# Performance work log

Measured on AMD Instinct MI355X. Metric: run time of the kernel, lower is better.

## Reference

```python
import jax, jax.numpy as jnp
import numpy as np

N, C, CI, H, W = 4, 512, 256, 64, 64  # batch, in_channels, inter_channels, spatial
EPS = 1e-5


def conv1x1(x, w, b):
    # x: (N,C,H,W), w: (O,C), b: (O,)
    return jnp.einsum('nchw,oc->nohw', x, w) + b[None, :, None, None]


def setup_inputs() -> dict:
    key = jax.random.key(0)
    ks = jax.random.split(key, 11)
    s = 0.02
    return {
        'x': jax.random.normal(ks[0], (N, C, H, W), dtype=jnp.float32),
        'g_w': jax.random.normal(ks[1], (CI, C), dtype=jnp.float32) * s,
        'g_b': jax.random.normal(ks[2], (CI,), dtype=jnp.float32) * s,
        'theta_w': jax.random.normal(ks[3], (CI, C), dtype=jnp.float32) * s,
        'theta_b': jax.random.normal(ks[4], (CI,), dtype=jnp.float32) * s,
        'phi_w': jax.random.normal(ks[5], (CI, C), dtype=jnp.float32) * s,
        'phi_b': jax.random.normal(ks[6], (CI,), dtype=jnp.float32) * s,
        'wz_w': jax.random.normal(ks[7], (C, CI), dtype=jnp.float32) * s,
        'wz_b': jax.random.normal(ks[8], (C,), dtype=jnp.float32) * s,
        'bn_gamma': jax.random.normal(ks[9], (C,), dtype=jnp.float32) * 0.1 + 1.0,
        'bn_beta': jax.random.normal(ks[10], (C,), dtype=jnp.float32) * 0.1,
    }


def reference(x, g_w, g_b, theta_w, theta_b, phi_w, phi_b, wz_w, wz_b, bn_gamma, bn_beta):
    # NLBlockND.forward_self, mode='embedded', dimension=2, bn_layer=True
    n = x.shape[0]
    L = x.shape[2] * x.shape[3]  # H*W tokens
    g_x = conv1x1(x, g_w, g_b).reshape(n, CI, L)          # (N,Ci,L)
    theta_x = conv1x1(x, theta_w, theta_b).reshape(n, CI, L)
    phi_x = conv1x1(x, phi_w, phi_b).reshape(n, CI, L)
    f = jnp.einsum('ncl,ncm->nlm', theta_x, phi_x)        # (N,L,L) = theta^T @ phi
    f_div_C = jax.nn.softmax(f, axis=-1)
    y = jnp.einsum('nlm,ncm->ncl', f_div_C, g_x)          # (N,Ci,L) = (attn @ g)^T
    y = y.reshape(n, CI, x.shape[2], x.shape[3])
    w_y = conv1x1(y, wz_w, wz_b)                          # (N,C,H,W)
    # BatchNorm2d, training-mode batch statistics (biased variance)
    mean = jnp.mean(w_y, axis=(0, 2, 3), keepdims=True)
    var = jnp.var(w_y, axis=(0, 2, 3), keepdims=True)
    w_y = (w_y - mean) * jax.lax.rsqrt(var + EPS)
    w_y = w_y * bn_gamma[None, :, None, None] + bn_beta[None, :, None, None]
    return w_y + x
```

## Files before the change

kernel.cpp:

```cpp
#include <hip/hip_runtime.h>
#include <hip/hip_bf16.h>
#include <hip/hip_fp16.h>


#define NB    4
#define CDIM  512
#define CIDIM 256
#define LDIM  4096
#define BN_EPS 1e-5f

typedef unsigned short u16;
typedef __attribute__((ext_vector_type(8))) short short8;
typedef __attribute__((ext_vector_type(4))) float f32x4;
typedef __attribute__((ext_vector_type(16))) float f32x16;

#define WY_OFF    0
#define THPH_OFF  8388608
#define G_OFF     12582912
#define Y_OFF     14680064
#define WTS_OFF   16777216
#define BIAS2_OFF 17039360
#define ML_OFF    17039872
#define ST_OFF    17105408

__device__ __forceinline__ u16 f2b(float f) {
    union { float f; unsigned u; } v; v.f = f;
    return (u16)((v.u + 0x7FFFu + ((v.u >> 16) & 1u)) >> 16);
}

__device__ __forceinline__ float b2f(u16 x) {
    return __uint_as_float((unsigned)x << 16);
}

__device__ __forceinline__ unsigned pack2(float a, float b) {
    return (unsigned)f2b(a) | ((unsigned)f2b(b) << 16);
}

__device__ __forceinline__ void gl_lds16(const u16* g, u16* l) {
    __builtin_amdgcn_global_load_lds(
        (const __attribute__((address_space(1))) void*)g,
        (__attribute__((address_space(3))) void*)l, 16, 0, 0);
}

__global__ void transpose_x(const float* __restrict__ x, u16* __restrict__ xt) {
    __shared__ float tile[32][33];
    int n = blockIdx.z;
    int l0 = blockIdx.x * 32, c0 = blockIdx.y * 32;
    const float* xn = x + (size_t)n * CDIM * LDIM;
    u16* xtn = xt + (size_t)n * LDIM * CDIM;
    int tx = threadIdx.x, ty = threadIdx.y;
#pragma unroll
    for (int k = 0; k < 4; k++)
        tile[ty + 8 * k][tx] = xn[(size_t)(c0 + ty + 8 * k) * LDIM + l0 + tx];
    __syncthreads();
#pragma unroll
    for (int k = 0; k < 4; k++)
        xtn[(size_t)(l0 + ty + 8 * k) * CDIM + c0 + tx] = f2b(tile[tx][ty + 8 * k]);
}

__global__ void cast_w(const float* __restrict__ gw, const float* __restrict__ tw,
                       const float* __restrict__ pw, const float* __restrict__ zw,
                       u16* __restrict__ out) {
    int idx = blockIdx.x * 256 + threadIdx.x;
    if (idx >= 4 * 131072) return;
    int seg = idx >> 17, off = idx & 131071;
    const float* s = (seg == 0) ? gw : (seg == 1) ? tw : (seg == 2) ? pw : zw;
    out[idx] = f2b(s[off]);
}

__global__ void concat_bias(const float* __restrict__ tb, const float* __restrict__ pb,
                            float* __restrict__ out) {
    int i = blockIdx.x * 256 + threadIdx.x;
    if (i < 256) out[i] = tb[i];
    else if (i < 512) out[i] = pb[i - 256];
}

template <int BIAS_MODE, bool OUT_BF16>
__global__ __launch_bounds__(256)
void gemm_nt(const u16* __restrict__ A, const u16* __restrict__ B,
             void* __restrict__ Dv, const float* __restrict__ bias,
             int K, int lda, int ldb, int ldd,
             long batchA, long batchB, long batchD) {
    __shared__ __align__(16) u16 As[128 * 32];
    __shared__ __align__(16) u16 Bs[128 * 32];
    int z = blockIdx.z;
    A += (size_t)z * batchA;
    B += (size_t)z * batchB;

    int tid = threadIdx.x, lane = tid & 63, wave = tid >> 6;
    int n0 = blockIdx.x * 128, m0 = blockIdx.y * 128;
    int wr = wave >> 1, wc = wave & 1;

    f32x4 acc[4][4];
#pragma unroll
    for (int i = 0; i < 4; i++)
#pragma unroll
        for (int j = 0; j < 4; j++) acc[i][j] = (f32x4){0.f, 0.f, 0.f, 0.f};

    int sr = wave * 16 + (lane >> 2);
    int ss = ((lane & 3) ^ ((lane >> 2) & 3)) * 8;
    const u16* Ag0 = A + (size_t)(m0 + sr) * lda + ss;
    const u16* Ag1 = A + (size_t)(m0 + 64 + sr) * lda + ss;
    const u16* Bg0 = B + (size_t)(n0 + sr) * ldb + ss;
    const u16* Bg1 = B + (size_t)(n0 + 64 + sr) * ldb + ss;
    u16* Al0 = &As[(wave * 16) * 32];
    u16* Al1 = &As[(64 + wave * 16) * 32];
    u16* Bl0 = &Bs[(wave * 16) * 32];
    u16* Bl1 = &Bs[(64 + wave * 16) * 32];

    int koff = ((lane >> 4) ^ (lane & 3)) * 8;
    int ra = (wr * 64 + (lane & 15)) * 32 + koff;
    int rb = (wc * 64 + (lane & 15)) * 32 + koff;

    for (int k0 = 0; k0 < K; k0 += 32) {
        __syncthreads();
        gl_lds16(Ag0 + k0, Al0);
        gl_lds16(Ag1 + k0, Al1);
        gl_lds16(Bg0 + k0, Bl0);
        gl_lds16(Bg1 + k0, Bl1);
        __syncthreads();

        short8 af[4], bf[4];
#pragma unroll
        for (int mt = 0; mt < 4; mt++) af[mt] = *(const short8*)&As[ra + mt * 16 * 32];
#pragma unroll
        for (int nt = 0; nt < 4; nt++) bf[nt] = *(const short8*)&Bs[rb + nt * 16 * 32];
#pragma unroll
        for (int mt = 0; mt < 4; mt++)
#pragma unroll
            for (int nt = 0; nt < 4; nt++)
                acc[mt][nt] = __builtin_amdgcn_mfma_f32_16x16x32_bf16(
                    af[mt], bf[nt], acc[mt][nt], 0, 0, 0);
    }

#pragma unroll
    for (int mt = 0; mt < 4; mt++) {
        int mg = m0 + wr * 64 + mt * 16 + (lane >> 4) * 4;
#pragma unroll
        for (int nt = 0; nt < 4; nt++) {
            int ng = n0 + wc * 64 + nt * 16 + (lane & 15);
#pragma unroll
            for (int r = 0; r < 4; r++) {
                float v = acc[mt][nt][r];
                if (BIAS_MODE == 1) v += bias[mg + r];
                if (BIAS_MODE == 2) v += bias[ng];
                if (OUT_BF16) {
                    u16* D = (u16*)Dv + (size_t)z * batchD;
                    D[(size_t)(mg + r) * ldd + ng] = f2b(v);
                } else {
                    float* D = (float*)Dv + (size_t)z * batchD;
                    D[(size_t)(mg + r) * ldd + ng] = v;
                }
            }
        }
    }
}

__global__ __launch_bounds__(256, 2)
void flash_attn(const u16* __restrict__ THPH, const u16* __restrict__ G,
                u16* __restrict__ OPB, unsigned* __restrict__ ML4) {
    __shared__ __align__(16) u16 Ks[2][32 * 256];
    __shared__ __align__(16) u16 Vs[2][256 * 32];

    int b = blockIdx.x;
    int n = b & 3;
    int jh = (b >> 2) & 3;
    int qt = b >> 4;
    int q0 = qt * 128;

    const u16* TH = THPH + (size_t)n * LDIM * 512;
    const u16* PH = TH + 256;
    const u16* Gn = G + (size_t)n * LDIM * CIDIM;
    u16* OPh = OPB + ((size_t)jh * NB + n) * CIDIM * LDIM;
    unsigned* MLh = ML4 + ((size_t)jh * NB + n) * LDIM;

    int tid = threadIdx.x, lane = tid & 63, w = tid >> 6;
    int h = lane >> 5, lq = lane & 31, l7 = lane & 7;

    short8 qf[16];
    {
        const u16* qb = TH + (size_t)(q0 + w * 32 + lq) * 512 + h * 8;
#pragma unroll
        for (int c = 0; c < 16; c++) qf[c] = *(const short8*)(qb + c * 16);
    }

    f32x16 o[8];
#pragma unroll
    for (int i = 0; i < 8; i++)
#pragma unroll
        for (int e = 0; e < 16; e++) o[i][e] = 0.f;
    float m = -3e38f, lsum = 0.f;

    int krh = lane >> 5;
    int ksl = lane & 31;
    int vr = lane >> 2;
    int vsl = (lane & 3) ^ ((lane >> 3) & 3);

#define STAGE(bufi, jt_) do {                                                  \
    int j0_ = jh * 1024 + (jt_) * 32;                                          \
    _Pragma("unroll")                                                          \
    for (int i = 0; i < 4; i++) {                                              \
        int r = w * 8 + 2 * i + krh;                                           \
        int s = ksl ^ (r & 7);                                                 \
        gl_lds16(PH + (size_t)(j0_ + r) * 512 + s * 8,                         \
                 &Ks[bufi][(w * 8 + 2 * i) * 256]);                            \
    }                                                                          \
    _Pragma("unroll")                                                          \
    for (int i = 0; i < 4; i++) {                                              \
        int r = w * 64 + 16 * i + vr;                                          \
        gl_lds16(Gn + (size_t)r * LDIM + j0_ + vsl * 8,                        \
                 &Vs[bufi][(w * 64 + 16 * i) * 32]);                           \
    }                                                                          \
} while (0)

    STAGE(0, 0);
    int cur = 0;

#pragma unroll 1
    for (int jt = 0; jt < 32; jt++) {
        __syncthreads();
        if (jt + 1 < 32) STAGE(cur ^ 1, jt + 1);

        const u16* kb = Ks[cur];
        const u16* vb = Vs[cur];

        f32x16 sv;
#pragma unroll
        for (int e = 0; e < 16; e++) sv[e] = 0.f;
#pragma unroll
        for (int c = 0; c < 16; c++) {
            int slot = (c * 2 + h) ^ l7;
            short8 ka = *(const short8*)&kb[lq * 256 + slot * 8];
            sv = __builtin_amdgcn_mfma_f32_32x32x16_bf16(ka, qf[c], sv, 0, 0, 0);
        }

        float tm = sv[0];
#pragma unroll
        for (int r = 1; r < 16; r++) tm = fmaxf(tm, sv[r]);
        tm = fmaxf(tm, __shfl_xor(tm, 32, 64));

        if (!__all(tm <= m + 8.0f)) {
            float mnew = fmaxf(m, tm);
            float al = __expf(m - mnew);
            m = mnew;
            lsum *= al;
#pragma unroll
            for (int i = 0; i < 8; i++)
#pragma unroll
                for (int e = 0; e < 16; e++) o[i][e] *= al;
        }

        float rs = 0.f;
#pragma unroll
        for (int r = 0; r < 16; r++) {
            float p = __expf(sv[r] - m);
            sv[r] = p;
            rs += p;
        }
        lsum += rs + __shfl_xor(rs, 32, 64);

#pragma unroll
        for (int st = 0; st < 2; st++) {
            int r0 = 8 * st;
            float e0 = sv[r0 + 0], e1 = sv[r0 + 1];
            float e2 = sv[r0 + 2], e3 = sv[r0 + 3];
            float e4 = sv[r0 + 4], e5 = sv[r0 + 5];
            float e6 = sv[r0 + 6], e7 = sv[r0 + 7];
            unsigned own_a = h ? pack2(e4, e5) : pack2(e0, e1);
            unsigned own_b = h ? pack2(e6, e7) : pack2(e2, e3);
            unsigned snd_a = h ? pack2(e0, e1) : pack2(e4, e5);
            unsigned snd_b = h ? pack2(e2, e3) : pack2(e6, e7);
            unsigned rcv_a = __shfl_xor(snd_a, 32, 64);
            unsigned rcv_b = __shfl_xor(snd_b, 32, 64);
            union { unsigned u[4]; short8 v; } pf;
            pf.u[0] = h ? rcv_a : own_a;
            pf.u[1] = h ? rcv_b : own_b;
            pf.u[2] = h ? own_a : rcv_a;
            pf.u[3] = h ? own_b : rcv_b;
#pragma unroll
            for (int cit = 0; cit < 8; cit++) {
                int row = cit * 32 + lq;
                int slot = (st * 2 + h) ^ ((lq >> 1) & 3);
                short8 va = *(const short8*)&vb[row * 32 + slot * 8];
                o[cit] = __builtin_amdgcn_mfma_f32_32x32x16_bf16(va, pf.v, o[cit], 0, 0, 0);
            }
        }
        cur ^= 1;
    }

    int q = q0 + w * 32 + lq;
    if (h == 0) {
        unsigned pm = (unsigned)__half_as_ushort(__float2half(m));
        unsigned pl = (unsigned)__half_as_ushort(__float2half(lsum));
        MLh[q] = pm | (pl << 16);
    }
#pragma unroll
    for (int cit = 0; cit < 8; cit++)
#pragma unroll
        for (int rr = 0; rr < 16; rr++) {
            int ci = cit * 32 + (rr & 3) + 8 * (rr >> 2) + 4 * h;
            OPh[(size_t)ci * LDIM + q] = f2b(o[cit][rr]);
        }
#undef STAGE
}

__global__ void merge_y(const u16* __restrict__ OPB, const unsigned* __restrict__ ML4,
                        u16* __restrict__ Y) {
    __shared__ u16 tile[32][33];
    int nn = blockIdx.z;
    int l0 = blockIdx.x * 32, ci0 = blockIdx.y * 32;
    int tx = threadIdx.x, ty = threadIdx.y;
    int l = l0 + tx;

    float mq[4], lq[4];
#pragma unroll
    for (int q = 0; q < 4; q++) {
        unsigned u = ML4[((size_t)q * NB + nn) * LDIM + l];
        mq[q] = __half2float(__ushort_as_half((unsigned short)(u & 0xffff)));
        lq[q] = __half2float(__ushort_as_half((unsigned short)(u >> 16)));
    }
    float M = fmaxf(fmaxf(mq[0], mq[1]), fmaxf(mq[2], mq[3]));
    float wq[4];
    float den = 0.f;
#pragma unroll
    for (int q = 0; q < 4; q++) {
        wq[q] = __expf(mq[q] - M);
        den += lq[q] * wq[q];
    }
    float inv = 1.f / den;
#pragma unroll
    for (int q = 0; q < 4; q++) wq[q] *= inv;

#pragma unroll
    for (int k = 0; k < 4; k++) {
        int ci = ci0 + ty + 8 * k;
        float acc = 0.f;
#pragma unroll
        for (int q = 0; q < 4; q++)
            acc += b2f(OPB[((size_t)q * NB + nn) * CIDIM * LDIM + (size_t)ci * LDIM + l]) * wq[q];
        tile[ty + 8 * k][tx] = f2b(acc);
    }
    __syncthreads();
    u16* Yn = Y + (size_t)nn * LDIM * CIDIM;
#pragma unroll
    for (int k = 0; k < 4; k++)
        Yn[(size_t)(l0 + ty + 8 * k) * CIDIM + ci0 + tx] = tile[tx][ty + 8 * k];
}

__global__ void bn_stats_kernel(const float* __restrict__ WY, float* __restrict__ stats) {
    int o = blockIdx.x, tid = threadIdx.x, lane = tid & 63, wave = tid >> 6;
    float s = 0.f, s2 = 0.f;
    for (int n = 0; n < NB; n++) {
        const float4* p = (const float4*)(WY + (size_t)(n * CDIM + o) * LDIM);
        for (int i = tid; i < LDIM / 4; i += 256) {
            float4 v = p[i];
            s += v.x + v.y + v.z + v.w;
            s2 += v.x * v.x + v.y * v.y + v.z * v.z + v.w * v.w;
        }
    }
    for (int o2 = 32; o2 > 0; o2 >>= 1) {
        s += __shfl_xor(s, o2, 64);
        s2 += __shfl_xor(s2, o2, 64);
    }
    __shared__ float rs[4], rs2[4];
    if (lane == 0) { rs[wave] = s; rs2[wave] = s2; }
    __syncthreads();
    if (tid == 0) {
        float S = rs[0] + rs[1] + rs[2] + rs[3];
        float S2 = rs2[0] + rs2[1] + rs2[2] + rs2[3];
        const float cnt = (float)(NB * LDIM);
        float mean = S / cnt;
        float var = S2 / cnt - mean * mean;
        stats[o] = mean;
        stats[CDIM + o] = rsqrtf(var + BN_EPS);
    }
}

__global__ void bn_apply_kernel(const float* __restrict__ WY, const float* __restrict__ stats,
                                const float* __restrict__ x,
                                const float* __restrict__ gamma, const float* __restrict__ beta,
                                float* __restrict__ out) {
    int i4 = blockIdx.x * 256 + threadIdx.x;
    int o = (i4 >> 10) & (CDIM - 1);
    float m = stats[o], is = stats[CDIM + o];
    float ga = gamma[o], be = beta[o];
    float4 w = ((const float4*)WY)[i4];
    float4 xv = ((const float4*)x)[i4];
    float4 r;
    r.x = (w.x - m) * is * ga + be + xv.x;
    r.y = (w.y - m) * is * ga + be + xv.y;
    r.z = (w.z - m) * is * ga + be + xv.z;
    r.w = (w.w - m) * is * ga + be + xv.w;
    ((float4*)out)[i4] = r;
}

extern "C" void kernel_launch(void* const* d_in, const int* in_sizes, int n_in,
                              void* d_out, int out_size, void* d_ws, size_t ws_size,
                              hipStream_t stream) {
    const float* x   = (const float*)d_in[0];
    const float* gw  = (const float*)d_in[1];
    const float* gb  = (const float*)d_in[2];
    const float* tw  = (const float*)d_in[3];
    const float* tb  = (const float*)d_in[4];
    const float* pw  = (const float*)d_in[5];
    const float* pb  = (const float*)d_in[6];
    const float* zw  = (const float*)d_in[7];
    const float* zb  = (const float*)d_in[8];
    const float* bng = (const float*)d_in[9];
    const float* bnb = (const float*)d_in[10];
    float* out = (float*)d_out;
    float* ws  = (float*)d_ws;

    float*    WY   = ws + WY_OFF;
    u16*      xT   = (u16*)(ws + WY_OFF);
    u16*      OPB  = (u16*)(ws + WY_OFF);
    u16*      THPH = (u16*)(ws + THPH_OFF);
    u16*      G    = (u16*)(ws + G_OFF);
    u16*      Y    = (u16*)(ws + Y_OFF);
    u16*      WB   = (u16*)(ws + WTS_OFF);
    float*    BC   = ws + BIAS2_OFF;
    unsigned* ML4  = (unsigned*)(ws + ML_OFF);
    float*    ST   = ws + ST_OFF;

    const long LC   = (long)LDIM * CDIM;
    const long LCI  = (long)LDIM * CIDIM;
    const long L512 = (long)LDIM * 512;
    const long CL   = (long)CDIM * LDIM;

    transpose_x<<<dim3(LDIM / 32, CDIM / 32, NB), dim3(32, 8), 0, stream>>>(x, xT);
    cast_w<<<2048, 256, 0, stream>>>(gw, tw, pw, zw, WB);
    concat_bias<<<2, 256, 0, stream>>>(tb, pb, BC);

    gemm_nt<2, true><<<dim3(4, 32, NB), 256, 0, stream>>>(
        xT, WB + 131072, THPH, BC, CDIM, CDIM, CDIM, 512, LC, 0, L512);
    gemm_nt<1, true><<<dim3(32, 2, NB), 256, 0, stream>>>(
        WB, xT, G, gb, CDIM, CDIM, CDIM, LDIM, 0, LC, LCI);

    flash_attn<<<dim3(512), 256, 0, stream>>>(THPH, G, OPB, ML4);
    merge_y<<<dim3(LDIM / 32, CIDIM / 32, NB), dim3(32, 8), 0, stream>>>(OPB, ML4, Y);

    gemm_nt<1, false><<<dim3(32, 4, NB), 256, 0, stream>>>(
        WB + 393216, Y, (void*)WY, zb, CIDIM, CIDIM, CIDIM, LDIM, 0, LCI, CL);

    bn_stats_kernel<<<dim3(CDIM), 256, 0, stream>>>(WY, ST);
    bn_apply_kernel<<<dim3(NB * CDIM * LDIM / 4 / 256), 256, 0, stream>>>(
        WY, ST, x, bng, bnb, out);
}
```

Before: 295.4 us.

## Software-pipeline attention loop: overlap next QK^T with current PV, use exp2

Restructures the flash-attention inner loop so the QK^T MFMA for the next key tile is issued alongside the PV MFMAs for the current tile, with the softmax for a tile computed ahead of time. s_setprio is raised around the MFMA block. LOG2E is folded into the theta weights and bias so exp2f can replace __expf, and the max and sum reductions become trees. This aims to hide the softmax VALU work and the LDS latency behind matrix-core work. It costs an extra 16-register score accumulator, adds register pressure, and changes the synchronisation pattern around the double buffers.

```diff
diff --git a/kernel.cpp b/kernel.cpp
--- a/kernel.cpp
+++ b/kernel.cpp
@@ -8,6 +8,7 @@
 #define CIDIM 256
 #define LDIM  4096
 #define BN_EPS 1e-5f
+#define LOG2E 1.4426950408889634f
 
 typedef unsigned short u16;
 typedef __attribute__((ext_vector_type(8))) short short8;
@@ -65,13 +66,15 @@
     if (idx >= 4 * 131072) return;
     int seg = idx >> 17, off = idx & 131071;
     const float* s = (seg == 0) ? gw : (seg == 1) ? tw : (seg == 2) ? pw : zw;
-    out[idx] = f2b(s[off]);
+    float v = s[off];
+    if (seg == 1) v *= LOG2E;
+    out[idx] = f2b(v);
 }
 
 __global__ void concat_bias(const float* __restrict__ tb, const float* __restrict__ pb,
                             float* __restrict__ out) {
     int i = blockIdx.x * 256 + threadIdx.x;
-    if (i < 256) out[i] = tb[i];
+    if (i < 256) out[i] = tb[i] * LOG2E;
     else if (i < 512) out[i] = pb[i - 256];
 }
 
@@ -213,80 +216,106 @@
     }                                                                          \
 } while (0)
 
+#define QKT(dst, bi) do {                                                      \
+    _Pragma("unroll")                                                          \
+    for (int e = 0; e < 16; e++) dst[e] = 0.f;                                 \
+    const u16* kb_ = Ks[bi];                                                   \
+    _Pragma("unroll")                                                          \
+    for (int c = 0; c < 16; c++) {                                             \
+        int slot = (c * 2 + h) ^ l7;                                           \
+        short8 ka = *(const short8*)&kb_[lq * 256 + slot * 8];                 \
+        dst = __builtin_amdgcn_mfma_f32_32x32x16_bf16(ka, qf[c], dst, 0, 0, 0);\
+    }                                                                          \
+} while (0)
+
+#define SOFTMAX_PACK(sv) do {                                                  \
+    float t01 = fmaxf(sv[0], sv[1]),   t23 = fmaxf(sv[2], sv[3]);              \
+    float t45 = fmaxf(sv[4], sv[5]),   t67 = fmaxf(sv[6], sv[7]);              \
+    float t89 = fmaxf(sv[8], sv[9]),   tab = fmaxf(sv[10], sv[11]);            \
+    float tcd = fmaxf(sv[12], sv[13]), tef = fmaxf(sv[14], sv[15]);            \
+    float u0 = fmaxf(t01, t23), u1 = fmaxf(t45, t67);                          \
+    float u2 = fmaxf(t89, tab), u3 = fmaxf(tcd, tef);                          \
+    float tm = fmaxf(fmaxf(u0, u1), fmaxf(u2, u3));                            \
+    tm = fmaxf(tm, __shfl_xor(tm, 32, 64));                                    \
+    if (!__all(tm <= m + 8.0f)) {                                              \
+        float mnew = fmaxf(m, tm);                                             \
+        float al = exp2f(m - mnew);                                            \
+        m = mnew;                                                              \
+        lsum *= al;                                                            \
+        _Pragma("unroll")                                                      \
+        for (int i = 0; i < 8; i++)                                            \
+            _Pragma("unroll")                                                  \
+            for (int e = 0; e < 16; e++) o[i][e] *= al;                        \
+    }                                                                          \
+    _Pragma("unroll")                                                          \
+    for (int r = 0; r < 16; r++) sv[r] = exp2f(sv[r] - m);                     \
+    float s0 = (sv[0] + sv[1]) + (sv[2] + sv[3]);                              \
+    float s1 = (sv[4] + sv[5]) + (sv[6] + sv[7]);                              \
+    float s2 = (sv[8] + sv[9]) + (sv[10] + sv[11]);                            \
+    float s3 = (sv[12] + sv[13]) + (sv[14] + sv[15]);                          \
+    float rs = (s0 + s1) + (s2 + s3);                                          \
+    lsum += rs + __shfl_xor(rs, 32, 64);                                       \
+    _Pragma("unroll")                                                          \
+    for (int st = 0; st < 2; st++) {                                           \
+        int r0 = 8 * st;                                                       \
+        float e0 = sv[r0 + 0], e1 = sv[r0 + 1];                                \
+        float e2 = sv[r0 + 2], e3 = sv[r0 + 3];                                \
+        float e4 = sv[r0 + 4], e5 = sv[r0 + 5];                                \
+        float e6 = sv[r0 + 6], e7 = sv[r0 + 7];                                \
+        unsigned own_a = h ? pack2(e4, e5) : pack2(e0, e1);                    \
+        unsigned own_b = h ? pack2(e6, e7) : pack2(e2, e3);                    \
+        unsigned snd_a = h ? pack2(e0, e1) : pack2(e4, e5);                    \
+        unsigned snd_b = h ? pack2(e2, e3) : pack2(e6, e7);                    \
+        unsigned rcv_a = __shfl_xor(snd_a, 32, 64);                            \
+        unsigned rcv_b = __shfl_xor(snd_b, 32, 64);                            \
+        unsigned* pu = st ? pf1 : pf0;                                         \
+        pu[0] = h ? rcv_a : own_a;                                             \
+        pu[1] = h ? rcv_b : own_b;                                             \
+        pu[2] = h ? own_a : rcv_a;                                             \
+        pu[3] = h ? own_b : rcv_b;                                             \
+    }                                                                          \
+} while (0)
+
+#define PV(bi) do {                                                            \
+    const u16* vb_ = Vs[bi];                                                   \
+    _Pragma("unroll")                                                          \
+    for (int st = 0; st < 2; st++) {                                           \
+        union { unsigned u[4]; short8 v; } pf;                                 \
+        unsigned* pu = st ? pf1 : pf0;                                         \
+        pf.u[0] = pu[0]; pf.u[1] = pu[1]; pf.u[2] = pu[2]; pf.u[3] = pu[3];    \
+        int slot = (st * 2 + h) ^ ((lq >> 1) & 3);                             \
+        _Pragma("unroll")                                                      \
+        for (int cit = 0; cit < 8; cit++) {                                    \
+            short8 va = *(const short8*)&vb_[(cit * 32 + lq) * 32 + slot * 8]; \
+            o[cit] = __builtin_amdgcn_mfma_f32_32x32x16_bf16(va, pf.v, o[cit], 0, 0, 0); \
+        }                                                                      \
+    }                                                                          \
+} while (0)
+
+    unsigned pf0[4], pf1[4];
+    f32x16 svA, svB;
+
     STAGE(0, 0);
-    int cur = 0;
+    __syncthreads();
+    STAGE(1, 1);
+    QKT(svA, 0);
 
 #pragma unroll 1
-    for (int jt = 0; jt < 32; jt++) {
+    for (int jt = 0; jt < 31; jt++) {
+        SOFTMAX_PACK(svA);
         __syncthreads();
-        if (jt + 1 < 32) STAGE(cur ^ 1, jt + 1);
-
-        const u16* kb = Ks[cur];
-        const u16* vb = Vs[cur];
-
-        f32x16 sv;
-#pragma unroll
-        for (int e = 0; e < 16; e++) sv[e] = 0.f;
-#pragma unroll
-        for (int c = 0; c < 16; c++) {
-            int slot = (c * 2 + h) ^ l7;
-            short8 ka = *(const short8*)&kb[lq * 256 + slot * 8];
-            sv = __builtin_amdgcn_mfma_f32_32x32x16_bf16(ka, qf[c], sv, 0, 0, 0);
+        __builtin_amdgcn_s_setprio(1);
+        QKT(svB, (jt + 1) & 1);
+        PV(jt & 1);
+        __builtin_amdgcn_s_setprio(0);
+        if (jt < 30) {
+            __syncthreads();
+            STAGE(jt & 1, jt + 2);
         }
-
-        float tm = sv[0];
-#pragma unroll
-        for (int r = 1; r < 16; r++) tm = fmaxf(tm, sv[r]);
-        tm = fmaxf(tm, __shfl_xor(tm, 32, 64));
-
-        if (!__all(tm <= m + 8.0f)) {
-            float mnew = fmaxf(m, tm);
-            float al = __expf(m - mnew);
-            m = mnew;
-            lsum *= al;
-#pragma unroll
-            for (int i = 0; i < 8; i++)
-#pragma unroll
-                for (int e = 0; e < 16; e++) o[i][e] *= al;
-        }
-
-        float rs = 0.f;
-#pragma unroll
-        for (int r = 0; r < 16; r++) {
-            float p = __expf(sv[r] - m);
-            sv[r] = p;
-            rs += p;
-        }
-        lsum += rs + __shfl_xor(rs, 32, 64);
-
-#pragma unroll
-        for (int st = 0; st < 2; st++) {
-            int r0 = 8 * st;
-            float e0 = sv[r0 + 0], e1 = sv[r0 + 1];
-            float e2 = sv[r0 + 2], e3 = sv[r0 + 3];
-            float e4 = sv[r0 + 4], e5 = sv[r0 + 5];
-            float e6 = sv[r0 + 6], e7 = sv[r0 + 7];
-            unsigned own_a = h ? pack2(e4, e5) : pack2(e0, e1);
-            unsigned own_b = h ? pack2(e6, e7) : pack2(e2, e3);
-            unsigned snd_a = h ? pack2(e0, e1) : pack2(e4, e5);
-            unsigned snd_b = h ? pack2(e2, e3) : pack2(e6, e7);
-            unsigned rcv_a = __shfl_xor(snd_a, 32, 64);
-            unsigned rcv_b = __shfl_xor(snd_b, 32, 64);
-            union { unsigned u[4]; short8 v; } pf;
-            pf.u[0] = h ? rcv_a : own_a;
-            pf.u[1] = h ? rcv_b : own_b;
-            pf.u[2] = h ? own_a : rcv_a;
-            pf.u[3] = h ? own_b : rcv_b;
-#pragma unroll
-            for (int cit = 0; cit < 8; cit++) {
-                int row = cit * 32 + lq;
-                int slot = (st * 2 + h) ^ ((lq >> 1) & 3);
-                short8 va = *(const short8*)&vb[row * 32 + slot * 8];
-                o[cit] = __builtin_amdgcn_mfma_f32_32x32x16_bf16(va, pf.v, o[cit], 0, 0, 0);
-            }
-        }
-        cur ^= 1;
-    }
+        svA = svB;
+    }
+    SOFTMAX_PACK(svA);
+    PV(1);
 
     int q = q0 + w * 32 + lq;
     if (h == 0) {
@@ -302,6 +331,9 @@
             OPh[(size_t)ci * LDIM + q] = f2b(o[cit][rr]);
         }
 #undef STAGE
+#undef QKT
+#undef SOFTMAX_PACK
+#undef PV
 }
 
 __global__ void merge_y(const u16* __restrict__ OPB, const unsigned* __restrict__ ML4,
@@ -324,7 +356,7 @@
     float den = 0.f;
 #pragma unroll
     for (int q = 0; q < 4; q++) {
-        wq[q] = __expf(mq[q] - M);
+        wq[q] = exp2f(mq[q] - M);
         den += lq[q] * wq[q];
     }
     float inv = 1.f / den;
```

After: 318.8 us. 1.08x slower.

## Fold log2e into theta weights, use exp2 in softmax, add MFMA priority hints

Applied to the files above, without the earlier changes.

Pre-scales theta weights and bias by log2(e) during the weight cast so the attention logits come out in base-2 units. The flash kernel and the merge kernel then use exp2f instead of __expf, which removes a multiply per exponential. The separate concat_bias launch is merged into cast_w, saving one kernel launch. It also raises wave priority around the MFMA loops with s_setprio and turns the max and sum reductions into trees to shorten dependency chains. The lazy-rescale threshold of 8 now applies in base-2 units, which changes when rescaling happens, and the bf16 rounding of the scaled weights shifts slightly.

```diff
diff --git a/kernel.cpp b/kernel.cpp
--- a/kernel.cpp
+++ b/kernel.cpp
@@ -8,6 +8,7 @@
 #define CIDIM 256
 #define LDIM  4096
 #define BN_EPS 1e-5f
+#define LOG2E 1.4426950408889634f
 
 typedef unsigned short u16;
 typedef __attribute__((ext_vector_type(8))) short short8;
@@ -60,19 +61,21 @@
 
 __global__ void cast_w(const float* __restrict__ gw, const float* __restrict__ tw,
                        const float* __restrict__ pw, const float* __restrict__ zw,
-                       u16* __restrict__ out) {
+                       u16* __restrict__ out,
+                       const float* __restrict__ tb, const float* __restrict__ pb,
+                       float* __restrict__ bc) {
     int idx = blockIdx.x * 256 + threadIdx.x;
-    if (idx >= 4 * 131072) return;
-    int seg = idx >> 17, off = idx & 131071;
-    const float* s = (seg == 0) ? gw : (seg == 1) ? tw : (seg == 2) ? pw : zw;
-    out[idx] = f2b(s[off]);
-}
-
-__global__ void concat_bias(const float* __restrict__ tb, const float* __restrict__ pb,
-                            float* __restrict__ out) {
-    int i = blockIdx.x * 256 + threadIdx.x;
-    if (i < 256) out[i] = tb[i];
-    else if (i < 512) out[i] = pb[i - 256];
+    if (idx < 4 * 131072) {
+        int seg = idx >> 17, off = idx & 131071;
+        const float* s = (seg == 0) ? gw : (seg == 1) ? tw : (seg == 2) ? pw : zw;
+        float v = s[off];
+        if (seg == 1) v *= LOG2E;
+        out[idx] = f2b(v);
+    } else {
+        int i = idx - 4 * 131072;
+        if (i < 256) bc[i] = tb[i] * LOG2E;
+        else if (i < 512) bc[i] = pb[i - 256];
+    }
 }
 
 template <int BIAS_MODE, bool OUT_BF16>
@@ -227,21 +230,27 @@
         f32x16 sv;
 #pragma unroll
         for (int e = 0; e < 16; e++) sv[e] = 0.f;
+        __builtin_amdgcn_s_setprio(1);
 #pragma unroll
         for (int c = 0; c < 16; c++) {
             int slot = (c * 2 + h) ^ l7;
             short8 ka = *(const short8*)&kb[lq * 256 + slot * 8];
             sv = __builtin_amdgcn_mfma_f32_32x32x16_bf16(ka, qf[c], sv, 0, 0, 0);
         }
-
-        float tm = sv[0];
-#pragma unroll
-        for (int r = 1; r < 16; r++) tm = fmaxf(tm, sv[r]);
+        __builtin_amdgcn_s_setprio(0);
+
+        float t01 = fmaxf(sv[0], sv[1]),   t23 = fmaxf(sv[2], sv[3]);
+        float t45 = fmaxf(sv[4], sv[5]),   t67 = fmaxf(sv[6], sv[7]);
+        float t89 = fmaxf(sv[8], sv[9]),   tab = fmaxf(sv[10], sv[11]);
+        float tcd = fmaxf(sv[12], sv[13]), tef = fmaxf(sv[14], sv[15]);
+        float u0 = fmaxf(t01, t23), u1 = fmaxf(t45, t67);
+        float u2 = fmaxf(t89, tab), u3 = fmaxf(tcd, tef);
+        float tm = fmaxf(fmaxf(u0, u1), fmaxf(u2, u3));
         tm = fmaxf(tm, __shfl_xor(tm, 32, 64));
 
         if (!__all(tm <= m + 8.0f)) {
             float mnew = fmaxf(m, tm);
-            float al = __expf(m - mnew);
+            float al = exp2f(m - mnew);
             m = mnew;
             lsum *= al;
 #pragma unroll
@@ -250,13 +259,13 @@
                 for (int e = 0; e < 16; e++) o[i][e] *= al;
         }
 
-        float rs = 0.f;
-#pragma unroll
-        for (int r = 0; r < 16; r++) {
-            float p = __expf(sv[r] - m);
-            sv[r] = p;
-            rs += p;
-        }
+#pragma unroll
+        for (int r = 0; r < 16; r++) sv[r] = exp2f(sv[r] - m);
+        float s0 = (sv[0] + sv[1]) + (sv[2] + sv[3]);
+        float s1 = (sv[4] + sv[5]) + (sv[6] + sv[7]);
+        float s2 = (sv[8] + sv[9]) + (sv[10] + sv[11]);
+        float s3 = (sv[12] + sv[13]) + (sv[14] + sv[15]);
+        float rs = (s0 + s1) + (s2 + s3);
         lsum += rs + __shfl_xor(rs, 32, 64);
 
 #pragma unroll
@@ -277,13 +286,14 @@
             pf.u[1] = h ? rcv_b : own_b;
             pf.u[2] = h ? own_a : rcv_a;
             pf.u[3] = h ? own_b : rcv_b;
+            int slot = (st * 2 + h) ^ ((lq >> 1) & 3);
+            __builtin_amdgcn_s_setprio(1);
 #pragma unroll
             for (int cit = 0; cit < 8; cit++) {
-                int row = cit * 32 + lq;
-                int slot = (st * 2 + h) ^ ((lq >> 1) & 3);
-                short8 va = *(const short8*)&vb[row * 32 + slot * 8];
+                short8 va = *(const short8*)&vb[(cit * 32 + lq) * 32 + slot * 8];
                 o[cit] = __builtin_amdgcn_mfma_f32_32x32x16_bf16(va, pf.v, o[cit], 0, 0, 0);
             }
+            __builtin_amdgcn_s_setprio(0);
         }
         cur ^= 1;
     }
@@ -324,7 +334,7 @@
     float den = 0.f;
 #pragma unroll
     for (int q = 0; q < 4; q++) {
-        wq[q] = __expf(mq[q] - M);
+        wq[q] = exp2f(mq[q] - M);
         den += lq[q] * wq[q];
     }
     float inv = 1.f / den;
@@ -428,8 +438,7 @@
     const long CL   = (long)CDIM * LDIM;
 
     transpose_x<<<dim3(LDIM / 32, CDIM / 32, NB), dim3(32, 8), 0, stream>>>(x, xT);
-    cast_w<<<2048, 256, 0, stream>>>(gw, tw, pw, zw, WB);
-    concat_bias<<<2, 256, 0, stream>>>(tb, pb, BC);
+    cast_w<<<2050, 256, 0, stream>>>(gw, tw, pw, zw, WB, tb, pb, BC);
 
     gemm_nt<2, true><<<dim3(4, 32, NB), 256, 0, stream>>>(
         xT, WB + 131072, THPH, BC, CDIM, CDIM, CDIM, 512, LC, 0, L512);
```

Result: slower. 302.5 us (+2.4%).
